# Kernel optimization log

Hardware: AMD Instinct MI355X
Metric: run time of the kernel (lower is better)

## Reference

```python
import jax, jax.numpy as jnp
import numpy as np

B, C_COMB, HW_IN, HW_FEAT, N_POS, D_PROJ, OUT_HW = 32, 448, 32, 64, 4096, 100, 256


def setup_inputs() -> dict:
    key = jax.random.key(0)
    k1, k2, k3, k4 = jax.random.split(key, 4)
    return {
        "combined": jax.random.normal(k1, (B, C_COMB, HW_IN, HW_IN), dtype=jnp.float32),
        "proj_w": jax.random.normal(k2, (D_PROJ, C_COMB), dtype=jnp.float32),
        "proj_b": jnp.zeros((D_PROJ,), dtype=jnp.float32),
        "mean": jax.random.normal(k3, (D_PROJ, N_POS), dtype=jnp.float32),
        "inv_covariance": jax.random.normal(k4, (N_POS, D_PROJ, D_PROJ), dtype=jnp.float32),
        "norm_min": jnp.zeros((), dtype=jnp.float32),
        "norm_max": jnp.ones((), dtype=jnp.float32),
    }


def reference(combined, proj_w, proj_b, mean, inv_covariance, norm_min, norm_max):
    b = combined.shape[0]
    # F.interpolate(..., size=(64,64), mode='bilinear', align_corners=False)
    feats = jax.image.resize(combined, (b, C_COMB, HW_FEAT, HW_FEAT), method="bilinear")
    # permute to NHWC and flatten spatial -> [B, 4096, 448]
    feats = feats.transpose(0, 2, 3, 1).reshape(b, N_POS, C_COMB)
    # nn.Linear(channels, 100) -> [B, 4096, 100]
    feats = jnp.einsum("bnc,dc->bnd", feats, proj_w) + proj_b
    # per-pixel Mahalanobis quadratic form: diff_n^T @ Sigma_n^{-1} @ diff_n
    diff = feats - mean.T[None]                                  # [B, 4096, 100]
    dist = jnp.einsum("bnc,ncd,bnd->bn", diff, inv_covariance, diff)  # [B, 4096]
    anomaly_map = dist.reshape(b, 1, HW_FEAT, HW_FEAT)
    anomaly_map = (anomaly_map - norm_min) / (norm_max - norm_min + 1e-8)
    anomaly_map = jax.image.resize(anomaly_map, (b, 1, OUT_HW, OUT_HW), method="bilinear")
    return anomaly_map
```

## Files before the change

### kernel.cpp

```cpp
#include <hip/hip_runtime.h>

#define B_      32
#define C_COMB  448
#define N_POS_  4096
#define D_      100

typedef __attribute__((ext_vector_type(8)))  short bf16x8;
typedef __attribute__((ext_vector_type(4)))  float f32x4;
typedef __attribute__((ext_vector_type(16))) float f32x16;

__device__ __forceinline__ unsigned short f2bf(float f) {
    unsigned u = __builtin_bit_cast(unsigned, f);
    u += 0x7FFFu + ((u >> 16) & 1u);
    return (unsigned short)(u >> 16);
}
__device__ __forceinline__ unsigned pack2bf(float a, float b) {
    return (unsigned)f2bf(a) | ((unsigned)f2bf(b) << 16);
}
__device__ __forceinline__ float bf2f(unsigned short h) {
    return __builtin_bit_cast(float, (unsigned)h << 16);
}
__device__ __forceinline__ float4 bf4_to_f4(uint2 u) {
    float4 r;
    r.x = __builtin_bit_cast(float, u.x << 16);
    r.y = __builtin_bit_cast(float, u.x & 0xffff0000u);
    r.z = __builtin_bit_cast(float, u.y << 16);
    r.w = __builtin_bit_cast(float, u.y & 0xffff0000u);
    return r;
}
__device__ __forceinline__ bf16x8 pack8bf(float4 lo, float4 hi) {
    bf16x8 r;
    r[0] = (short)f2bf(lo.x); r[1] = (short)f2bf(lo.y);
    r[2] = (short)f2bf(lo.z); r[3] = (short)f2bf(lo.w);
    r[4] = (short)f2bf(hi.x); r[5] = (short)f2bf(hi.y);
    r[6] = (short)f2bf(hi.z); r[7] = (short)f2bf(hi.w);
    return r;
}

__device__ __forceinline__ void gl_lds16(const float* g, float* l) {
    __builtin_amdgcn_global_load_lds(
        (const __attribute__((address_space(1))) void*)g,
        (__attribute__((address_space(3))) void*)l, 16, 0, 0);
}

__global__ __launch_bounds__(256) void k_prep(const float* __restrict__ W,
                                              unsigned short* __restrict__ Wb) {
    int i = blockIdx.x * 256 + threadIdx.x;
    if (i < 11200) {
        float4 v = ((const float4*)W)[i];
        ((uint2*)Wb)[i] = make_uint2(pack2bf(v.x, v.y), pack2bf(v.z, v.w));
    }
}

__global__ __launch_bounds__(256) void k_proj(const float* __restrict__ comb,
                                              const unsigned short* __restrict__ Wb,
                                              const float* __restrict__ bias,
                                              unsigned short* __restrict__ p32b) {
    __shared__ float Tf[32 * 65];
    __shared__ unsigned short Ws[D_ * 40];

    const int pt = blockIdx.x, b = blockIdx.y;
    const int t = threadIdx.x;
    const int lane = t & 63, w = t >> 6;
    const int c = lane & 15, q = lane >> 4;

    f32x4 acc[7];
#pragma unroll
    for (int mt = 0; mt < 7; mt++) acc[mt] = (f32x4){0.f, 0.f, 0.f, 0.f};

    const float4* comb4 = (const float4*)comb;

    for (int kt = 0; kt < 14; kt++) {
        __syncthreads();
#pragma unroll
        for (int k = 0; k < 2; k++) {
            int e4 = t + 256 * k;
            int cc = e4 >> 4, p4 = e4 & 15;
            float4 v = comb4[((size_t)b * C_COMB + kt * 32 + cc) * 256 + pt * 16 + p4];
            Tf[cc * 65 + p4 * 4 + 0] = v.x;
            Tf[cc * 65 + p4 * 4 + 1] = v.y;
            Tf[cc * 65 + p4 * 4 + 2] = v.z;
            Tf[cc * 65 + p4 * 4 + 3] = v.w;
        }
#pragma unroll
        for (int k = 0; k < 4; k++) {
            int e = t + 256 * k;
            if (e < 800) {
                int d = e >> 3, c4 = e & 7;
                *(uint2*)(Ws + d * 40 + c4 * 4) =
                    *(const uint2*)(Wb + d * C_COMB + kt * 32 + c4 * 4);
            }
        }
        __syncthreads();

        bf16x8 bfrag;
#pragma unroll
        for (int j = 0; j < 8; j++) {
            bfrag[j] = (short)f2bf(Tf[(q * 8 + j) * 65 + w * 16 + c]);
        }
#pragma unroll
        for (int mt = 0; mt < 7; mt++) {
            int r = mt * 16 + c;
            bf16x8 afrag;
            if (r < D_) afrag = *(const bf16x8*)(Ws + r * 40 + q * 8);
            else        afrag = (bf16x8){0,0,0,0,0,0,0,0};
            acc[mt] = __builtin_amdgcn_mfma_f32_16x16x32_bf16(afrag, bfrag, acc[mt], 0, 0, 0);
        }
    }

    const int pos = pt * 64 + w * 16 + c;
#pragma unroll
    for (int mt = 0; mt < 7; mt++) {
        int d0 = mt * 16 + q * 4;
        if (d0 < D_) {
            f32x4 a = acc[mt];
            float o0 = a[0] + bias[d0 + 0];
            float o1 = a[1] + bias[d0 + 1];
            float o2 = a[2] + bias[d0 + 2];
            float o3 = a[3] + bias[d0 + 3];
            *(uint2*)(p32b + ((size_t)pos * B_ + b) * D_ + d0) =
                make_uint2(pack2bf(o0, o1), pack2bf(o2, o3));
        }
    }
}

__global__ __launch_bounds__(256) void k_mahal(const unsigned short* __restrict__ p32b,
                                               const float* __restrict__ mean,
                                               const float* __restrict__ icov,
                                               float* __restrict__ gdist) {
    __shared__ float icovL[10000];
    __shared__ unsigned short dTb[B_ * 104];
    __shared__ float meanL[112];
    __shared__ float part[128];

    const int n = blockIdx.x;
    const int t = threadIdx.x;
    const int lane = t & 63, w = t >> 6;
    const int half = lane >> 5;
    const int l31  = lane & 31;

    const float* Msrc = icov + (size_t)n * (D_ * D_);
    {
        const int wbase = w * 64;
#pragma unroll
        for (int it = 0; it < 9; it++) {
            int idx = it * 256 + t;
            gl_lds16(Msrc + (size_t)idx * 4, icovL + (it * 256 + wbase) * 4);
        }
        int idx = 9 * 256 + t;
        if (idx < 2500) {
            gl_lds16(Msrc + (size_t)idx * 4, icovL + (9 * 256 + wbase) * 4);
        }
    }

    if (t < 100) meanL[t] = mean[t * N_POS_ + n];
    if (t >= 128 && t < 160) *(uint2*)(dTb + (t - 128) * 104 + 100) = make_uint2(0u, 0u);

    const int y = n >> 6, x = n & 63;
    float sy = 0.5f * y - 0.25f, sx = 0.5f * x - 0.25f;
    float y0f = floorf(sy), x0f = floorf(sx);
    float fy = sy - y0f, fx = sx - x0f;
    int iy0 = max((int)y0f, 0), iy1 = min((int)y0f + 1, 31);
    int ix0 = max((int)x0f, 0), ix1 = min((int)x0f + 1, 31);
    const float w00 = (1.f - fy) * (1.f - fx), w01 = (1.f - fy) * fx;
    const float w10 = fy * (1.f - fx),         w11 = fy * fx;
    const unsigned short* s00 = p32b + (size_t)(iy0 * 32 + ix0) * 3200;
    const unsigned short* s01 = p32b + (size_t)(iy0 * 32 + ix1) * 3200;
    const unsigned short* s10 = p32b + (size_t)(iy1 * 32 + ix0) * 3200;
    const unsigned short* s11 = p32b + (size_t)(iy1 * 32 + ix1) * 3200;

    __syncthreads();

#pragma unroll
    for (int k = 0; k < 4; k++) {
        int e4 = t + 256 * k;
        if (e4 < 800) {
            int b  = e4 / 25;
            int d4 = e4 - b * 25;
            float4 f00 = bf4_to_f4(*(const uint2*)(s00 + e4 * 4));
            float4 f01 = bf4_to_f4(*(const uint2*)(s01 + e4 * 4));
            float4 f10 = bf4_to_f4(*(const uint2*)(s10 + e4 * 4));
            float4 f11 = bf4_to_f4(*(const uint2*)(s11 + e4 * 4));
            float4 m = *(const float4*)(meanL + d4 * 4);
            float vx = w00 * f00.x + w01 * f01.x + w10 * f10.x + w11 * f11.x - m.x;
            float vy = w00 * f00.y + w01 * f01.y + w10 * f10.y + w11 * f11.y - m.y;
            float vz = w00 * f00.z + w01 * f01.z + w10 * f10.z + w11 * f11.z - m.z;
            float vw = w00 * f00.w + w01 * f01.w + w10 * f10.w + w11 * f11.w - m.w;
            *(uint2*)(dTb + b * 104 + d4 * 4) =
                make_uint2(pack2bf(vx, vy), pack2bf(vz, vw));
        }
    }
    __syncthreads();

    const int r = 32 * w + l31;
    const bool rv = (r < D_);
    const float* MrowL = icovL + r * D_;

    f32x16 acc = {0.f,0.f,0.f,0.f,0.f,0.f,0.f,0.f,0.f,0.f,0.f,0.f,0.f,0.f,0.f,0.f};
#pragma unroll
    for (int kt = 0; kt < 7; kt++) {
        int k0 = kt * 16 + half * 8;
        bf16x8 afrag;
        if (rv && k0 < D_) {
            float4 lo = *(const float4*)(MrowL + k0);
            float4 hi;
            if (k0 + 4 < D_) hi = *(const float4*)(MrowL + k0 + 4);
            else             hi = (float4){0.f, 0.f, 0.f, 0.f};
            afrag = pack8bf(lo, hi);
        } else {
            afrag = (bf16x8){0,0,0,0,0,0,0,0};
        }
        bf16x8 bfrag;
        if (k0 < D_) bfrag = *(const bf16x8*)(dTb + l31 * 104 + k0);
        else         bfrag = (bf16x8){0,0,0,0,0,0,0,0};
        acc = __builtin_amdgcn_mfma_f32_32x32x16_bf16(afrag, bfrag, acc, 0, 0, 0);
    }

    float dist = 0.f;
#pragma unroll
    for (int reg = 0; reg < 16; reg++) {
        int rr = 32 * w + (reg & 3) + 8 * (reg >> 2) + 4 * half;
        if (rr < D_) dist += acc[reg] * bf2f(dTb[l31 * 104 + rr]);
    }
    dist += __shfl_xor(dist, 32);
    if (half == 0) part[w * 32 + l31] = dist;
    __syncthreads();
    if (t < 32) {
        float s = part[t] + part[32 + t] + part[64 + t] + part[96 + t];
        gdist[t * N_POS_ + n] = s;
    }
}

__global__ __launch_bounds__(256) void k_upsample(const float* __restrict__ gdist,
                                                  const float* __restrict__ nminp,
                                                  const float* __restrict__ nmaxp,
                                                  float* __restrict__ out) {
    int gid = blockIdx.x * 256 + threadIdx.x;
    int b   = gid >> 16;
    int rem = gid & 65535;
    int Y = rem >> 8, X = rem & 255;
    float sy = 0.25f * Y - 0.375f, sx = 0.25f * X - 0.375f;
    float y0f = floorf(sy), x0f = floorf(sx);
    float fy = sy - y0f, fx = sx - x0f;
    int iy0 = max((int)y0f, 0), iy1 = min((int)y0f + 1, 63);
    int ix0 = max((int)x0f, 0), ix1 = min((int)x0f + 1, 63);
    const float* g = gdist + b * N_POS_;
    float v00 = g[iy0 * 64 + ix0], v01 = g[iy0 * 64 + ix1];
    float v10 = g[iy1 * 64 + ix0], v11 = g[iy1 * 64 + ix1];
    float v = (1.f - fy) * ((1.f - fx) * v00 + fx * v01)
            +        fy  * ((1.f - fx) * v10 + fx * v11);
    float nmin = nminp[0], nmax = nmaxp[0];
    float scale = 1.0f / (nmax - nmin + 1e-8f);
    out[gid] = (v - nmin) * scale;
}

extern "C" void kernel_launch(void* const* d_in, const int* in_sizes, int n_in,
                              void* d_out, int out_size, void* d_ws, size_t ws_size,
                              hipStream_t stream) {
    const float* comb = (const float*)d_in[0];
    const float* W    = (const float*)d_in[1];
    const float* bias = (const float*)d_in[2];
    const float* mean = (const float*)d_in[3];
    const float* icov = (const float*)d_in[4];
    const float* nmin = (const float*)d_in[5];
    const float* nmax = (const float*)d_in[6];
    float* out = (float*)d_out;

    char* ws = (char*)d_ws;
    unsigned short* p32b  = (unsigned short*)(ws);
    unsigned short* Wb    = (unsigned short*)(ws + 6553600);
    float*          gdist = (float*)(ws + 6643200);

    k_prep    <<<44, 256, 0, stream>>>(W, Wb);
    k_proj    <<<dim3(16, 32), 256, 0, stream>>>(comb, Wb, bias, p32b);
    k_mahal   <<<4096, 256, 0, stream>>>(p32b, mean, icov, gdist);
    k_upsample<<<8192, 256, 0, stream>>>(gdist, nmin, nmax, out);
}
```

Measured before the change: 306.2 us.

## Double-buffer projection staging, fold weight conversion into proj, reorder mahal loads

```diff
diff --git a/kernel.cpp b/kernel.cpp
--- a/kernel.cpp
+++ b/kernel.cpp
@@ -43,21 +43,12 @@
         (__attribute__((address_space(3))) void*)l, 16, 0, 0);
 }
 
-__global__ __launch_bounds__(256) void k_prep(const float* __restrict__ W,
-                                              unsigned short* __restrict__ Wb) {
-    int i = blockIdx.x * 256 + threadIdx.x;
-    if (i < 11200) {
-        float4 v = ((const float4*)W)[i];
-        ((uint2*)Wb)[i] = make_uint2(pack2bf(v.x, v.y), pack2bf(v.z, v.w));
-    }
-}
-
 __global__ __launch_bounds__(256) void k_proj(const float* __restrict__ comb,
-                                              const unsigned short* __restrict__ Wb,
+                                              const float* __restrict__ W,
                                               const float* __restrict__ bias,
                                               unsigned short* __restrict__ p32b) {
-    __shared__ float Tf[32 * 65];
-    __shared__ unsigned short Ws[D_ * 40];
+    __shared__ float Tf[2][32 * 64];
+    __shared__ unsigned short Ws[2][D_ * 32];
 
     const int pt = blockIdx.x, b = blockIdx.y;
     const int t = threadIdx.x;
@@ -70,42 +61,55 @@
 
     const float4* comb4 = (const float4*)comb;
 
-    for (int kt = 0; kt < 14; kt++) {
-        __syncthreads();
+    auto stage_comb = [&](int kt, int buf) {
 #pragma unroll
         for (int k = 0; k < 2; k++) {
-            int e4 = t + 256 * k;
+            int e4 = k * 256 + t;
             int cc = e4 >> 4, p4 = e4 & 15;
-            float4 v = comb4[((size_t)b * C_COMB + kt * 32 + cc) * 256 + pt * 16 + p4];
-            Tf[cc * 65 + p4 * 4 + 0] = v.x;
-            Tf[cc * 65 + p4 * 4 + 1] = v.y;
-            Tf[cc * 65 + p4 * 4 + 2] = v.z;
-            Tf[cc * 65 + p4 * 4 + 3] = v.w;
-        }
+            const float* src = (const float*)(comb4 +
+                ((size_t)(b * C_COMB + kt * 32 + cc) * 256 + pt * 16 + p4));
+            float* dst = &Tf[buf][0] + (size_t)(k * 256 + w * 64) * 4;
+            gl_lds16(src, dst);
+        }
+    };
+    auto stage_W = [&](int kt, int buf) {
 #pragma unroll
         for (int k = 0; k < 4; k++) {
             int e = t + 256 * k;
             if (e < 800) {
                 int d = e >> 3, c4 = e & 7;
-                *(uint2*)(Ws + d * 40 + c4 * 4) =
-                    *(const uint2*)(Wb + d * C_COMB + kt * 32 + c4 * 4);
+                float4 v = *(const float4*)(W + (size_t)d * C_COMB + kt * 32 + c4 * 4);
+                *(uint2*)(&Ws[buf][0] + d * 32 + c4 * 4) =
+                    make_uint2(pack2bf(v.x, v.y), pack2bf(v.z, v.w));
             }
         }
-        __syncthreads();
-
+    };
+
+    stage_comb(0, 0);
+    stage_W(0, 0);
+    __syncthreads();
+
+    int cur = 0;
+    for (int kt = 0; kt < 14; kt++) {
+        if (kt < 13) {
+            stage_comb(kt + 1, cur ^ 1);
+            stage_W(kt + 1, cur ^ 1);
+        }
         bf16x8 bfrag;
 #pragma unroll
         for (int j = 0; j < 8; j++) {
-            bfrag[j] = (short)f2bf(Tf[(q * 8 + j) * 65 + w * 16 + c]);
+            bfrag[j] = (short)f2bf(Tf[cur][(q * 8 + j) * 64 + w * 16 + c]);
         }
 #pragma unroll
         for (int mt = 0; mt < 7; mt++) {
             int r = mt * 16 + c;
             bf16x8 afrag;
-            if (r < D_) afrag = *(const bf16x8*)(Ws + r * 40 + q * 8);
+            if (r < D_) afrag = *(const bf16x8*)(&Ws[cur][0] + r * 32 + q * 8);
             else        afrag = (bf16x8){0,0,0,0,0,0,0,0};
             acc[mt] = __builtin_amdgcn_mfma_f32_16x16x32_bf16(afrag, bfrag, acc[mt], 0, 0, 0);
         }
+        __syncthreads();
+        cur ^= 1;
     }
 
     const int pos = pt * 64 + w * 16 + c;
@@ -130,7 +134,6 @@
                                                float* __restrict__ gdist) {
     __shared__ float icovL[10000];
     __shared__ unsigned short dTb[B_ * 104];
-    __shared__ float meanL[112];
     __shared__ float part[128];
 
     const int n = blockIdx.x;
@@ -138,23 +141,6 @@
     const int lane = t & 63, w = t >> 6;
     const int half = lane >> 5;
     const int l31  = lane & 31;
-
-    const float* Msrc = icov + (size_t)n * (D_ * D_);
-    {
-        const int wbase = w * 64;
-#pragma unroll
-        for (int it = 0; it < 9; it++) {
-            int idx = it * 256 + t;
-            gl_lds16(Msrc + (size_t)idx * 4, icovL + (it * 256 + wbase) * 4);
-        }
-        int idx = 9 * 256 + t;
-        if (idx < 2500) {
-            gl_lds16(Msrc + (size_t)idx * 4, icovL + (9 * 256 + wbase) * 4);
-        }
-    }
-
-    if (t < 100) meanL[t] = mean[t * N_POS_ + n];
-    if (t >= 128 && t < 160) *(uint2*)(dTb + (t - 128) * 104 + 100) = make_uint2(0u, 0u);
 
     const int y = n >> 6, x = n & 63;
     float sy = 0.5f * y - 0.25f, sx = 0.5f * x - 0.25f;
@@ -169,19 +155,50 @@
     const unsigned short* s10 = p32b + (size_t)(iy1 * 32 + ix0) * 3200;
     const unsigned short* s11 = p32b + (size_t)(iy1 * 32 + ix1) * 3200;
 
-    __syncthreads();
-
+    uint2 u00[4], u01[4], u10[4], u11[4];
+    float4 mv[4];
+#pragma unroll
+    for (int k = 0; k < 4; k++) {
+        int e4 = t + 256 * k;
+        if (e4 < 800) {
+            int d4 = e4 - (e4 / 25) * 25;
+            u00[k] = *(const uint2*)(s00 + e4 * 4);
+            u01[k] = *(const uint2*)(s01 + e4 * 4);
+            u10[k] = *(const uint2*)(s10 + e4 * 4);
+            u11[k] = *(const uint2*)(s11 + e4 * 4);
+            mv[k].x = mean[(size_t)(d4 * 4 + 0) * N_POS_ + n];
+            mv[k].y = mean[(size_t)(d4 * 4 + 1) * N_POS_ + n];
+            mv[k].z = mean[(size_t)(d4 * 4 + 2) * N_POS_ + n];
+            mv[k].w = mean[(size_t)(d4 * 4 + 3) * N_POS_ + n];
+        }
+    }
+
+    const float* Msrc = icov + (size_t)n * (D_ * D_);
+    {
+        const int wbase = w * 64;
+#pragma unroll
+        for (int it = 0; it < 9; it++) {
+            int idx = it * 256 + t;
+            gl_lds16(Msrc + (size_t)idx * 4, icovL + (it * 256 + wbase) * 4);
+        }
+        int idx = 9 * 256 + t;
+        if (idx < 2500) {
+            gl_lds16(Msrc + (size_t)idx * 4, icovL + (9 * 256 + wbase) * 4);
+        }
+    }
+
+    if (t >= 128 && t < 160) *(uint2*)(dTb + (t - 128) * 104 + 100) = make_uint2(0u, 0u);
 #pragma unroll
     for (int k = 0; k < 4; k++) {
         int e4 = t + 256 * k;
         if (e4 < 800) {
             int b  = e4 / 25;
             int d4 = e4 - b * 25;
-            float4 f00 = bf4_to_f4(*(const uint2*)(s00 + e4 * 4));
-            float4 f01 = bf4_to_f4(*(const uint2*)(s01 + e4 * 4));
-            float4 f10 = bf4_to_f4(*(const uint2*)(s10 + e4 * 4));
-            float4 f11 = bf4_to_f4(*(const uint2*)(s11 + e4 * 4));
-            float4 m = *(const float4*)(meanL + d4 * 4);
+            float4 f00 = bf4_to_f4(u00[k]);
+            float4 f01 = bf4_to_f4(u01[k]);
+            float4 f10 = bf4_to_f4(u10[k]);
+            float4 f11 = bf4_to_f4(u11[k]);
+            float4 m = mv[k];
             float vx = w00 * f00.x + w01 * f01.x + w10 * f10.x + w11 * f11.x - m.x;
             float vy = w00 * f00.y + w01 * f01.y + w10 * f10.y + w11 * f11.y - m.y;
             float vz = w00 * f00.z + w01 * f01.z + w10 * f10.z + w11 * f11.z - m.z;
@@ -268,11 +285,9 @@
 
     char* ws = (char*)d_ws;
     unsigned short* p32b  = (unsigned short*)(ws);
-    unsigned short* Wb    = (unsigned short*)(ws + 6553600);
-    float*          gdist = (float*)(ws + 6643200);
-
-    k_prep    <<<44, 256, 0, stream>>>(W, Wb);
-    k_proj    <<<dim3(16, 32), 256, 0, stream>>>(comb, Wb, bias, p32b);
+    float*          gdist = (float*)(ws + 6553600);
+
+    k_proj    <<<dim3(16, 32), 256, 0, stream>>>(comb, W, bias, p32b);
     k_mahal   <<<4096, 256, 0, stream>>>(p32b, mean, icov, gdist);
     k_upsample<<<8192, 256, 0, stream>>>(gdist, nmin, nmax, out);
 }
```

Result: slower. 313.4 us (+2.4%).
